# Kernel optimization log

Measured on AMD Instinct MI355X. Metric: run time of the kernel, lower is better.

The kernel has to match this reference:

```python
import jax, jax.numpy as jnp
import numpy as np

PATCH = 2
NW = 4  # n_wires -> 2**4 = 16-dim state


def _rx(t):
    c = jnp.cos(t / 2).astype(jnp.complex64)
    s = (-1j * jnp.sin(t / 2)).astype(jnp.complex64)
    return jnp.stack([jnp.stack([c, s]), jnp.stack([s, c])])


def _ry(t):
    c = jnp.cos(t / 2)
    s = jnp.sin(t / 2)
    return jnp.stack([jnp.stack([c, -s]), jnp.stack([s, c])]).astype(jnp.complex64)


def _rz(t):
    e = jnp.exp(-0.5j * t.astype(jnp.complex64))
    z = jnp.zeros((), jnp.complex64)
    return jnp.stack([jnp.stack([e, z]), jnp.stack([z, jnp.conj(e)])])


def _apply_1q(state, U, w):
    # state: (N,2,2,2,2); apply 2x2 gate U on wire w
    state = jnp.moveaxis(state, 1 + w, -1)
    state = state @ U.T
    return jnp.moveaxis(state, -1, 1 + w)


def _apply_cnot(state, c, t):
    state = jnp.moveaxis(state, (1 + c, 1 + t), (-2, -1))
    flipped = state[..., ::-1]  # X on target
    state = jnp.concatenate([state[..., 0:1, :], flipped[..., 1:2, :]], axis=-2)
    return jnp.moveaxis(state, (-2, -1), (1 + c, 1 + t))


def setup_inputs() -> dict:
    key = jax.random.key(0)
    k1, k2 = jax.random.split(key)
    x = jax.random.normal(k1, (128, 1, 128, 128), dtype=jnp.float32)
    # fixed RandomLayer rotation angles (6 parametrized gates out of 8 ops)
    layer_params = jax.random.uniform(k2, (6,), dtype=jnp.float32, minval=0.0, maxval=2.0 * np.pi)
    return {"x": x, "layer_params": layer_params}


def reference(x, layer_params):
    B, _, H, W = x.shape
    nh, nw = H // PATCH, W // PATCH
    N = B * nh * nw
    # extract 2x2 patches in row-major (r outer, c inner) order, flattened row-major
    ang = x[:, 0].reshape(B, nh, PATCH, nw, PATCH).transpose(0, 1, 3, 2, 4).reshape(N, 4)
    # RY(theta) on |0> per wire -> product state
    half = ang / 2
    amps = jnp.stack([jnp.cos(half), jnp.sin(half)], axis=-1).astype(jnp.complex64)  # (N,4,2)
    state = jnp.einsum('na,nb,nc,nd->nabcd', amps[:, 0], amps[:, 1], amps[:, 2], amps[:, 3])
    # fixed random layer: 8 ops = 6 rotations + 2 CNOTs
    t = layer_params
    state = _apply_1q(state, _rx(t[0]), 0)
    state = _apply_1q(state, _ry(t[1]), 1)
    state = _apply_1q(state, _rz(t[2]), 2)
    state = _apply_cnot(state, 0, 2)
    state = _apply_1q(state, _rx(t[3]), 3)
    state = _apply_1q(state, _ry(t[4]), 0)
    state = _apply_cnot(state, 1, 3)
    state = _apply_1q(state, _rz(t[5]), 2)
    # <Z_w> expectation per wire
    p = state.real ** 2 + state.imag ** 2  # (N,2,2,2,2)
    z = jnp.array([1.0, -1.0], dtype=p.dtype)
    meas = jnp.stack(
        [jnp.tensordot(p, z, axes=([1 + w], [0])).sum(axis=(1, 2, 3)) for w in range(NW)],
        axis=-1,
    )  # (N,4)
    return meas.reshape(B, nh * nw * NW)
```

## Files before the change

### kernel.cpp

```cpp
#include <hip/hip_runtime.h>
#include <math.h>

__global__ __launch_bounds__(256) void qfe_kernel(
    const float* __restrict__ x, const float* __restrict__ tp,
    float* __restrict__ out, int N)
{
    int n = blockIdx.x * blockDim.x + threadIdx.x;
    if (n >= N) return;

    int b   = n >> 12;
    int rem = n & 4095;
    int pi  = rem >> 6;
    int pj  = rem & 63;

    const float* base = x + ((size_t)b << 14) + (pi << 8) + (pj << 1);
    float2 r0 = *reinterpret_cast<const float2*>(base);
    float2 r1 = *reinterpret_cast<const float2*>(base + 128);

    float A[4][2];
    {
        float ang[4] = {r0.x, r0.y, r1.x, r1.y};
        #pragma unroll
        for (int w = 0; w < 4; ++w) {
            float s, c;
            sincosf(0.5f * ang[w], &s, &c);
            A[w][0] = c; A[w][1] = s;
        }
    }

    float re[16], im[16];
    #pragma unroll
    for (int i = 0; i < 16; ++i) {
        re[i] = A[0][(i >> 3) & 1] * A[1][(i >> 2) & 1]
              * A[2][(i >> 1) & 1] * A[3][i & 1];
        im[i] = 0.0f;
    }

    float gc[6], gs[6];
    #pragma unroll
    for (int k = 0; k < 6; ++k) {
        float s, c;
        sincosf(0.5f * tp[k], &s, &c);
        gc[k] = c; gs[k] = s;
    }

    auto apply_rx = [&](int m, float c, float s) {
        #pragma unroll
        for (int i = 0; i < 16; ++i) {
            if (i & m) continue;
            int j = i | m;
            float r0_ = re[i], i0_ = im[i], r1_ = re[j], i1_ = im[j];
            re[i] =  c * r0_ + s * i1_;
            im[i] =  c * i0_ - s * r1_;
            re[j] =  s * i0_ + c * r1_;
            im[j] = -s * r0_ + c * i1_;
        }
    };
    auto apply_ry = [&](int m, float c, float s) {
        #pragma unroll
        for (int i = 0; i < 16; ++i) {
            if (i & m) continue;
            int j = i | m;
            float r0_ = re[i], i0_ = im[i], r1_ = re[j], i1_ = im[j];
            re[i] = c * r0_ - s * r1_;
            im[i] = c * i0_ - s * i1_;
            re[j] = s * r0_ + c * r1_;
            im[j] = s * i0_ + c * i1_;
        }
    };
    auto apply_rz = [&](int m, float c, float s) {
        #pragma unroll
        for (int i = 0; i < 16; ++i) {
            float r_ = re[i], i_ = im[i];
            if (i & m) { re[i] = c * r_ - s * i_; im[i] = c * i_ + s * r_; }
            else       { re[i] = c * r_ + s * i_; im[i] = c * i_ - s * r_; }
        }
    };
    auto apply_cnot = [&](int cm, int tm) {
        #pragma unroll
        for (int i = 0; i < 16; ++i) {
            if ((i & cm) && !(i & tm)) {
                int j = i | tm;
                float tr = re[i]; re[i] = re[j]; re[j] = tr;
                float ti = im[i]; im[i] = im[j]; im[j] = ti;
            }
        }
    };

    apply_rx(8, gc[0], gs[0]);
    apply_ry(4, gc[1], gs[1]);
    apply_rz(2, gc[2], gs[2]);
    apply_cnot(8, 2);
    apply_rx(1, gc[3], gs[3]);
    apply_ry(8, gc[4], gs[4]);
    apply_cnot(4, 1);
    apply_rz(2, gc[5], gs[5]);

    float m0 = 0.f, m1 = 0.f, m2 = 0.f, m3 = 0.f;
    #pragma unroll
    for (int i = 0; i < 16; ++i) {
        float p = re[i] * re[i] + im[i] * im[i];
        m0 += (i & 8) ? -p : p;
        m1 += (i & 4) ? -p : p;
        m2 += (i & 2) ? -p : p;
        m3 += (i & 1) ? -p : p;
    }

    *reinterpret_cast<float4*>(out + ((size_t)n << 2)) = make_float4(m0, m1, m2, m3);
}

extern "C" void kernel_launch(void* const* d_in, const int* in_sizes, int n_in,
                              void* d_out, int out_size, void* d_ws, size_t ws_size,
                              hipStream_t stream) {
    const float* x  = (const float*)d_in[0];
    const float* tp = (const float*)d_in[1];
    float* out = (float*)d_out;

    int N = in_sizes[0] / 4;
    const int threads = 256;
    int blocks = (N + threads - 1) / threads;
    qfe_kernel<<<blocks, threads, 0, stream>>>(x, tp, out, N);
}
```

Before: 70.91 us.

## Replace statevector simulation with closed-form Pauli-Z expectation formulas

Derives each wire's <Z> expectation analytically from the fixed circuit and evaluates it directly from trig values of the input angles and gate parameters. This drops the 16-amplitude complex state, the gate sweeps and the probability reduction. It also switches to fast intrinsics (__sincosf/__cosf), which trades accuracy for speed. The kernel is memory-bound at this size, so the gain is limited by global loads and stores.

```diff
diff --git a/kernel.cpp b/kernel.cpp
--- a/kernel.cpp
+++ b/kernel.cpp
@@ -8,6 +8,14 @@
     int n = blockIdx.x * blockDim.x + threadIdx.x;
     if (n >= N) return;
 
+    float c0 = __cosf(tp[0]);
+    float s1, c1; __sincosf(tp[1], &s1, &c1);
+    float c2 = __cosf(tp[2]);
+    float c3 = __cosf(tp[3]);
+    float s4, c4; __sincosf(tp[4], &s4, &c4);
+    float k00 = c0 * c4;
+    float k01 = c2 * s4;
+
     int b   = n >> 12;
     int rem = n & 4095;
     int pi  = rem >> 6;
@@ -17,94 +25,16 @@
     float2 r0 = *reinterpret_cast<const float2*>(base);
     float2 r1 = *reinterpret_cast<const float2*>(base + 128);
 
-    float A[4][2];
-    {
-        float ang[4] = {r0.x, r0.y, r1.x, r1.y};
-        #pragma unroll
-        for (int w = 0; w < 4; ++w) {
-            float s, c;
-            sincosf(0.5f * ang[w], &s, &c);
-            A[w][0] = c; A[w][1] = s;
-        }
-    }
+    float sa0, ca0; __sincosf(r0.x, &sa0, &ca0);
+    float sa1, ca1; __sincosf(r0.y, &sa1, &ca1);
+    float sa2, ca2; __sincosf(r1.x, &sa2, &ca2);
+    float ca3 = __cosf(r1.y);
 
-    float re[16], im[16];
-    #pragma unroll
-    for (int i = 0; i < 16; ++i) {
-        re[i] = A[0][(i >> 3) & 1] * A[1][(i >> 2) & 1]
-              * A[2][(i >> 1) & 1] * A[3][i & 1];
-        im[i] = 0.0f;
-    }
-
-    float gc[6], gs[6];
-    #pragma unroll
-    for (int k = 0; k < 6; ++k) {
-        float s, c;
-        sincosf(0.5f * tp[k], &s, &c);
-        gc[k] = c; gs[k] = s;
-    }
-
-    auto apply_rx = [&](int m, float c, float s) {
-        #pragma unroll
-        for (int i = 0; i < 16; ++i) {
-            if (i & m) continue;
-            int j = i | m;
-            float r0_ = re[i], i0_ = im[i], r1_ = re[j], i1_ = im[j];
-            re[i] =  c * r0_ + s * i1_;
-            im[i] =  c * i0_ - s * r1_;
-            re[j] =  s * i0_ + c * r1_;
-            im[j] = -s * r0_ + c * i1_;
-        }
-    };
-    auto apply_ry = [&](int m, float c, float s) {
-        #pragma unroll
-        for (int i = 0; i < 16; ++i) {
-            if (i & m) continue;
-            int j = i | m;
-            float r0_ = re[i], i0_ = im[i], r1_ = re[j], i1_ = im[j];
-            re[i] = c * r0_ - s * r1_;
-            im[i] = c * i0_ - s * i1_;
-            re[j] = s * r0_ + c * r1_;
-            im[j] = s * i0_ + c * i1_;
-        }
-    };
-    auto apply_rz = [&](int m, float c, float s) {
-        #pragma unroll
-        for (int i = 0; i < 16; ++i) {
-            float r_ = re[i], i_ = im[i];
-            if (i & m) { re[i] = c * r_ - s * i_; im[i] = c * i_ + s * r_; }
-            else       { re[i] = c * r_ + s * i_; im[i] = c * i_ - s * r_; }
-        }
-    };
-    auto apply_cnot = [&](int cm, int tm) {
-        #pragma unroll
-        for (int i = 0; i < 16; ++i) {
-            if ((i & cm) && !(i & tm)) {
-                int j = i | tm;
-                float tr = re[i]; re[i] = re[j]; re[j] = tr;
-                float ti = im[i]; im[i] = im[j]; im[j] = ti;
-            }
-        }
-    };
-
-    apply_rx(8, gc[0], gs[0]);
-    apply_ry(4, gc[1], gs[1]);
-    apply_rz(2, gc[2], gs[2]);
-    apply_cnot(8, 2);
-    apply_rx(1, gc[3], gs[3]);
-    apply_ry(8, gc[4], gs[4]);
-    apply_cnot(4, 1);
-    apply_rz(2, gc[5], gs[5]);
-
-    float m0 = 0.f, m1 = 0.f, m2 = 0.f, m3 = 0.f;
-    #pragma unroll
-    for (int i = 0; i < 16; ++i) {
-        float p = re[i] * re[i] + im[i] * im[i];
-        m0 += (i & 8) ? -p : p;
-        m1 += (i & 4) ? -p : p;
-        m2 += (i & 2) ? -p : p;
-        m3 += (i & 1) ? -p : p;
-    }
+    float u  = c1 * ca1 - s1 * sa1;
+    float m0 = k00 * ca0 - k01 * (sa0 * sa2);
+    float m1 = u;
+    float m2 = c0 * (ca0 * ca2);
+    float m3 = c3 * (u * ca3);
 
     *reinterpret_cast<float4*>(out + ((size_t)n << 2)) = make_float4(m0, m1, m2, m3);
 }
```

Result: faster. 60.36 us (-14.9%).
